# Kernel optimization log

Hardware: AMD Instinct MI355X
Metric: run time of the kernel (lower is better)

The kernel has to match this reference:

```python
import jax, jax.numpy as jnp
import numpy as np

GROUP_NUM = 4
NODE_NUM = 4096
FEAT_DIM = 128
THRESHOLD = 0.6


def setup_inputs() -> dict:
    key = jax.random.key(0)
    # kaiming-uniform-ish init for the learned bridge-node features
    bound = np.sqrt(6.0 / FEAT_DIM)  # fan_in = feat_dim
    nodes = jax.random.uniform(key, (GROUP_NUM, NODE_NUM, FEAT_DIM),
                               dtype=jnp.float32, minval=-bound, maxval=bound)
    return {"nodes": nodes}


def reference(nodes):
    # Per group g: sim = sigmoid(nodes_g @ nodes_g.T); adj = where(sim < t, 0, sim)
    # [g, n, f] x [g, m, f] -> [g, n, m]
    node_dot = jnp.einsum('gnf,gmf->gnm', nodes, nodes)
    node_sim = jax.nn.sigmoid(node_dot)
    inner_adj = jnp.where(node_sim < THRESHOLD, jnp.zeros((), node_sim.dtype), node_sim)
    # edge_index = inner_adj.nonzero() in the original is data-dependent stream
    # compaction; the dense weighted adjacency carries the same information.
    return inner_adj
```

## Files before the change

### kernel.cpp

```cpp
#include <hip/hip_runtime.h>
#include <math.h>


constexpr int GROUPS = 4;
constexpr int N = 4096;
constexpr int F = 128;
constexpr int BT = 64;
constexpr int KS = 32;
constexpr int TILES = N / BT;
constexpr int PAIRS = TILES * (TILES + 1) / 2;
constexpr int TPAD = 68;
constexpr float THRESH = 0.6f;

__device__ __forceinline__ int row_start(int r) { return r * TILES - (r * (r - 1)) / 2; }

__global__ __launch_bounds__(512, 8)
void bridge_nodes_kernel(const float* __restrict__ nodes, float* __restrict__ out) {
    __shared__ float Bs[BT * KS];
    __shared__ float T[BT * TPAD];

    const int g = blockIdx.y;
    const int t = blockIdx.x;

    int bm = (int)((2 * TILES + 1
                    - sqrtf((float)((2 * TILES + 1) * (2 * TILES + 1) - 8 * t))) * 0.5f);
    bm = bm < 0 ? 0 : (bm > TILES - 1 ? TILES - 1 : bm);
    while (row_start(bm) > t) --bm;
    while (row_start(bm + 1) <= t) ++bm;
    const int bn = bm + (t - row_start(bm));

    const float* __restrict__ base = nodes + (size_t)g * N * F;
    const int tid  = threadIdx.x;
    const int lane = tid & 63;
    const int wrow = __builtin_amdgcn_readfirstlane((tid >> 6) * 8);
    const float* __restrict__ Arow = base + (size_t)(bm * BT + wrow) * F;

    const int srow = tid >> 3;
    const int skq  = tid & 7;
    const float* __restrict__ Bld = base + (size_t)(bn * BT + srow) * F + skq * 4;
    float4* BsG = (float4*)Bs;
    const int wgran = srow * 8 + (skq ^ (srow & 7));

    float acc[8] = {0.f, 0.f, 0.f, 0.f, 0.f, 0.f, 0.f, 0.f};

    float4 bv = *(const float4*)(Bld);
#pragma unroll
    for (int kc = 0; kc < F / KS; ++kc) {
        const int kb = kc * KS;
        __syncthreads();
        BsG[wgran] = bv;
        __syncthreads();
        if (kc < F / KS - 1)
            bv = *(const float4*)(Bld + (kb + KS));

        float4 breg[8];
#pragma unroll
        for (int q = 0; q < 8; ++q)
            breg[q] = BsG[lane * 8 + (q ^ (lane & 7))];

#pragma unroll
        for (int q = 0; q < 8; ++q) {
            float4 a[8];
#pragma unroll
            for (int r = 0; r < 8; ++r)
                a[r] = *(const float4*)(Arow + r * F + kb + q * 4);
            const float4 b = breg[q];
#pragma unroll
            for (int r = 0; r < 8; ++r) acc[r] = fmaf(a[r].x, b.x, acc[r]);
#pragma unroll
            for (int r = 0; r < 8; ++r) acc[r] = fmaf(a[r].y, b.y, acc[r]);
#pragma unroll
            for (int r = 0; r < 8; ++r) acc[r] = fmaf(a[r].z, b.z, acc[r]);
#pragma unroll
            for (int r = 0; r < 8; ++r) acc[r] = fmaf(a[r].w, b.w, acc[r]);
        }
    }

#pragma unroll
    for (int r = 0; r < 8; ++r) {
        const float s = 1.0f / (1.0f + expf(-acc[r]));
        acc[r] = (s < THRESH) ? 0.0f : s;
    }

    const size_t outg = (size_t)g * N * N;
    {
        float* o = out + outg + (size_t)(bm * BT + wrow) * N + bn * BT + lane;
#pragma unroll
        for (int r = 0; r < 8; ++r) o[(size_t)r * N] = acc[r];
    }

    if (bm != bn) {
        float4 t0 = {acc[0], acc[1], acc[2], acc[3]};
        float4 t1 = {acc[4], acc[5], acc[6], acc[7]};
        *(float4*)&T[lane * TPAD + wrow]     = t0;
        *(float4*)&T[lane * TPAD + wrow + 4] = t1;
        __syncthreads();
        const int mr = tid >> 3;
        const int qc = (tid & 7) * 8;
        const float4 v0 = *(const float4*)&T[mr * TPAD + qc];
        const float4 v1 = *(const float4*)&T[mr * TPAD + qc + 4];
        float* o = out + outg + (size_t)(bn * BT + mr) * N + bm * BT + qc;
        *(float4*)o = v0;
        *(float4*)(o + 4) = v1;
    }
}

extern "C" void kernel_launch(void* const* d_in, const int* in_sizes, int n_in,
                              void* d_out, int out_size, void* d_ws, size_t ws_size,
                              hipStream_t stream) {
    const float* nodes = (const float*)d_in[0];
    float* out = (float*)d_out;
    dim3 grid(PAIRS, GROUPS);
    dim3 block(512);
    bridge_nodes_kernel<<<grid, block, 0, stream>>>(nodes, out);
}
```

Measured before the change: 385.3 us.

## Use bf16 MFMA for symmetric Gram tiles with FP32 fixup near threshold

Converts the node features to bf16 in a pre-pass and computes the symmetric Gram tiles with 16x16x32 bf16 MFMA instructions on 128x128 tiles, loading operands into swizzled LDS through global_load_lds. Entries whose logit lands within a narrow band of the threshold logit are appended to a workspace list with an atomic counter. A fixup kernel then recomputes those entries in full FP32 so the thresholded output still matches the reference. This replaces the FP32 FMA inner loop and its LDS transposes with matrix-core work. It adds two extra launches and an atomic hot spot, and correctness depends on the band being wide enough to cover bf16 error and on the list capacity not overflowing.

```diff
diff --git a/kernel.cpp b/kernel.cpp
--- a/kernel.cpp
+++ b/kernel.cpp
@@ -5,23 +5,47 @@
 constexpr int GROUPS = 4;
 constexpr int N = 4096;
 constexpr int F = 128;
-constexpr int BT = 64;
-constexpr int KS = 32;
+constexpr int BT = 128;
 constexpr int TILES = N / BT;
 constexpr int PAIRS = TILES * (TILES + 1) / 2;
-constexpr int TPAD = 68;
 constexpr float THRESH = 0.6f;
+constexpr float LOGIT = 0.405465108f;
+constexpr float BAND = 0.006f;
+
+constexpr size_t H_OFF_SHORTS = 8;
+constexpr size_t H_ELEMS = (size_t)GROUPS * N * F;
+
+using short8 = __attribute__((ext_vector_type(8))) short;
+using f32x4  = __attribute__((ext_vector_type(4))) float;
 
 __device__ __forceinline__ int row_start(int r) { return r * TILES - (r * (r - 1)) / 2; }
 
-__global__ __launch_bounds__(512, 8)
-void bridge_nodes_kernel(const float* __restrict__ nodes, float* __restrict__ out) {
-    __shared__ float Bs[BT * KS];
-    __shared__ float T[BT * TPAD];
+__device__ __forceinline__ short f2bf_rne(float x) {
+    unsigned u = __float_as_uint(x);
+    return (short)((u + 0x7FFFu + ((u >> 16) & 1u)) >> 16);
+}
+
+__global__ void split_kernel(const float* __restrict__ in, short* __restrict__ h,
+                             unsigned* __restrict__ cnt) {
+    const int i = blockIdx.x * 256 + threadIdx.x;
+    if (i == 0) *cnt = 0;
+    if (i < (int)H_ELEMS) h[i] = f2bf_rne(in[i]);
+}
+
+#define GLL16(gp, lp)                                                        \
+    __builtin_amdgcn_global_load_lds(                                        \
+        (const __attribute__((address_space(1))) void*)(gp),                 \
+        (__attribute__((address_space(3))) void*)(lp), 16, 0, 0)
+
+__global__ __launch_bounds__(256, 2)
+void bridge_mfma_kernel(const short* __restrict__ W, float* __restrict__ out,
+                        unsigned* __restrict__ cnt, unsigned* __restrict__ list,
+                        unsigned cap) {
+    __shared__ alignas(16) short ldsA[BT * F];
+    __shared__ alignas(16) short ldsB[BT * F];
 
     const int g = blockIdx.y;
     const int t = blockIdx.x;
-
     int bm = (int)((2 * TILES + 1
                     - sqrtf((float)((2 * TILES + 1) * (2 * TILES + 1) - 8 * t))) * 0.5f);
     bm = bm < 0 ? 0 : (bm > TILES - 1 ? TILES - 1 : bm);
@@ -29,79 +53,114 @@
     while (row_start(bm + 1) <= t) ++bm;
     const int bn = bm + (t - row_start(bm));
 
-    const float* __restrict__ base = nodes + (size_t)g * N * F;
     const int tid  = threadIdx.x;
     const int lane = tid & 63;
-    const int wrow = __builtin_amdgcn_readfirstlane((tid >> 6) * 8);
-    const float* __restrict__ Arow = base + (size_t)(bm * BT + wrow) * F;
+    const int wv   = tid >> 6;
+    const int lm   = lane & 15;
+    const int q    = lane >> 4;
+    const int R    = (wv & 1) * 64;
+    const int C    = (wv >> 1) * 64;
 
-    const int srow = tid >> 3;
-    const int skq  = tid & 7;
-    const float* __restrict__ Bld = base + (size_t)(bn * BT + srow) * F + skq * 4;
-    float4* BsG = (float4*)Bs;
-    const int wgran = srow * 8 + (skq ^ (srow & 7));
-
-    float acc[8] = {0.f, 0.f, 0.f, 0.f, 0.f, 0.f, 0.f, 0.f};
-
-    float4 bv = *(const float4*)(Bld);
-#pragma unroll
-    for (int kc = 0; kc < F / KS; ++kc) {
-        const int kb = kc * KS;
-        __syncthreads();
-        BsG[wgran] = bv;
-        __syncthreads();
-        if (kc < F / KS - 1)
-            bv = *(const float4*)(Bld + (kb + KS));
-
-        float4 breg[8];
-#pragma unroll
-        for (int q = 0; q < 8; ++q)
-            breg[q] = BsG[lane * 8 + (q ^ (lane & 7))];
+    const short* baseA = W + ((size_t)g * N + bm * BT) * F;
+    const short* baseB = W + ((size_t)g * N + bn * BT) * F;
 
 #pragma unroll
-        for (int q = 0; q < 8; ++q) {
-            float4 a[8];
+    for (int it = 0; it < 8; ++it) {
+        const int g0 = tid + 256 * it;
+        const int r  = g0 >> 4;
+        const int o  = g0 & 15;
+        const int so = o ^ (r & 15);
+        GLL16(baseA + (size_t)r * F + so * 8, &ldsA[g0 * 8]);
+        GLL16(baseB + (size_t)r * F + so * 8, &ldsB[g0 * 8]);
+    }
+    __syncthreads();
+
+    f32x4 acc[4][4] = {};
 #pragma unroll
-            for (int r = 0; r < 8; ++r)
-                a[r] = *(const float4*)(Arow + r * F + kb + q * 4);
-            const float4 b = breg[q];
+    for (int kc = 0; kc < 4; ++kc) {
+        short8 af[4], bf[4];
 #pragma unroll
-            for (int r = 0; r < 8; ++r) acc[r] = fmaf(a[r].x, b.x, acc[r]);
+        for (int i = 0; i < 4; ++i) {
+            const int row = R + i * 16 + lm;
+            af[i] = *(const short8*)(ldsA + row * 16 * 8 + (((kc * 4 + q) ^ lm) * 8));
+        }
 #pragma unroll
-            for (int r = 0; r < 8; ++r) acc[r] = fmaf(a[r].y, b.y, acc[r]);
+        for (int j = 0; j < 4; ++j) {
+            const int row = C + j * 16 + lm;
+            bf[j] = *(const short8*)(ldsB + row * 16 * 8 + (((kc * 4 + q) ^ lm) * 8));
+        }
 #pragma unroll
-            for (int r = 0; r < 8; ++r) acc[r] = fmaf(a[r].z, b.z, acc[r]);
+        for (int i = 0; i < 4; ++i)
 #pragma unroll
-            for (int r = 0; r < 8; ++r) acc[r] = fmaf(a[r].w, b.w, acc[r]);
-        }
-    }
-
-#pragma unroll
-    for (int r = 0; r < 8; ++r) {
-        const float s = 1.0f / (1.0f + expf(-acc[r]));
-        acc[r] = (s < THRESH) ? 0.0f : s;
+            for (int j = 0; j < 4; ++j)
+                acc[i][j] = __builtin_amdgcn_mfma_f32_16x16x32_bf16(
+                    af[i], bf[j], acc[i][j], 0, 0, 0);
     }
 
     const size_t outg = (size_t)g * N * N;
-    {
-        float* o = out + outg + (size_t)(bm * BT + wrow) * N + bn * BT + lane;
+    float val[4][4][4];
 #pragma unroll
-        for (int r = 0; r < 8; ++r) o[(size_t)r * N] = acc[r];
-    }
+    for (int i = 0; i < 4; ++i)
+#pragma unroll
+        for (int j = 0; j < 4; ++j)
+#pragma unroll
+            for (int r = 0; r < 4; ++r) {
+                const float x = acc[i][j][r];
+                const float e = __expf(-x);
+                const float s = __builtin_amdgcn_rcpf(1.0f + e);
+                val[i][j][r] = (s < THRESH) ? 0.0f : s;
+                if (fabsf(x - LOGIT) < BAND) {
+                    const unsigned row = bm * BT + R + i * 16 + q * 4 + r;
+                    const unsigned col = bn * BT + C + j * 16 + lm;
+                    const unsigned idx = atomicAdd(cnt, 1u);
+                    if (idx < cap)
+                        list[idx] = ((unsigned)g << 24) | (row << 12) | col;
+                }
+            }
+
+#pragma unroll
+    for (int i = 0; i < 4; ++i)
+#pragma unroll
+        for (int r = 0; r < 4; ++r) {
+            const int row = bm * BT + R + i * 16 + q * 4 + r;
+            float* o = out + outg + (size_t)row * N + bn * BT + C;
+#pragma unroll
+            for (int j = 0; j < 4; ++j)
+                o[j * 16 + lm] = val[i][j][r];
+        }
 
     if (bm != bn) {
-        float4 t0 = {acc[0], acc[1], acc[2], acc[3]};
-        float4 t1 = {acc[4], acc[5], acc[6], acc[7]};
-        *(float4*)&T[lane * TPAD + wrow]     = t0;
-        *(float4*)&T[lane * TPAD + wrow + 4] = t1;
-        __syncthreads();
-        const int mr = tid >> 3;
-        const int qc = (tid & 7) * 8;
-        const float4 v0 = *(const float4*)&T[mr * TPAD + qc];
-        const float4 v1 = *(const float4*)&T[mr * TPAD + qc + 4];
-        float* o = out + outg + (size_t)(bn * BT + mr) * N + bm * BT + qc;
-        *(float4*)o = v0;
-        *(float4*)(o + 4) = v1;
+#pragma unroll
+        for (int j = 0; j < 4; ++j) {
+            const int mrow = bn * BT + C + j * 16 + lm;
+            float* o = out + outg + (size_t)mrow * N + bm * BT + R;
+#pragma unroll
+            for (int i = 0; i < 4; ++i) {
+                float4 v = {val[i][j][0], val[i][j][1], val[i][j][2], val[i][j][3]};
+                *(float4*)(o + i * 16 + q * 4) = v;
+            }
+        }
+    }
+}
+
+__global__ void fixup_kernel(const float* __restrict__ nodes, float* __restrict__ out,
+                             const unsigned* __restrict__ cnt,
+                             const unsigned* __restrict__ list, unsigned cap) {
+    unsigned n = *cnt;
+    if (n > cap) n = cap;
+    const unsigned stride = gridDim.x * blockDim.x;
+    for (unsigned idx = blockIdx.x * blockDim.x + threadIdx.x; idx < n; idx += stride) {
+        const unsigned p = list[idx];
+        const unsigned g = p >> 24, row = (p >> 12) & 0xFFF, col = p & 0xFFF;
+        const float* a = nodes + ((size_t)g * N + row) * F;
+        const float* b = nodes + ((size_t)g * N + col) * F;
+        float acc = 0.0f;
+        for (int k = 0; k < F; ++k)
+            acc = fmaf(a[k], b[k], acc);
+        const float s = 1.0f / (1.0f + expf(-acc));
+        const float v = (s < THRESH) ? 0.0f : s;
+        out[(size_t)g * N * N + (size_t)row * N + col] = v;
+        out[(size_t)g * N * N + (size_t)col * N + row] = v;
     }
 }
 
@@ -110,7 +169,19 @@
                               hipStream_t stream) {
     const float* nodes = (const float*)d_in[0];
     float* out = (float*)d_out;
+
+    unsigned* cnt = (unsigned*)d_ws;
+    short* h = (short*)d_ws + H_OFF_SHORTS;
+    const size_t list_off_bytes = 16 + H_ELEMS * sizeof(short);
+    unsigned* list = (unsigned*)((char*)d_ws + list_off_bytes);
+    const size_t cap_sz = (ws_size > list_off_bytes + 16)
+                              ? (ws_size - list_off_bytes) / sizeof(unsigned) : 0;
+    const unsigned cap = (unsigned)(cap_sz > (1u << 22) ? (1u << 22) : cap_sz);
+
+    split_kernel<<<(int)((H_ELEMS + 255) / 256), 256, 0, stream>>>(nodes, h, cnt);
+
     dim3 grid(PAIRS, GROUPS);
-    dim3 block(512);
-    bridge_nodes_kernel<<<grid, block, 0, stream>>>(nodes, out);
+    bridge_mfma_kernel<<<grid, 256, 0, stream>>>(h, out, cnt, list, cap);
+
+    fixup_kernel<<<512, 256, 0, stream>>>(nodes, out, cnt, list, cap);
 }
```

Result: slower. 978.6 us (+154.0%).
